# Kernel tuning notes

Measured on AMD Instinct MI355X. Metric: run time of the kernel, lower is better.

The kernel has to match this reference:

```python
import jax, jax.numpy as jnp
import numpy as np

N, E, IN_DIM, HID, TOWERS, NG = 20000, 320000, 16, 50, 5, 64
FO = HID // TOWERS  # out channels per tower = 10
EPS_BN = 1e-5
EPS_STD = 1e-5  # PyG StdAggregation: sqrt(relu(var) + 1e-5)


def setup_inputs() -> dict:
    key = jax.random.key(0)
    ks = jax.random.split(key, 24)
    rn = lambda k, shape: jax.random.normal(k, shape, dtype=jnp.float32) * 0.1
    F0, F1 = IN_DIM, HID
    return {
        "x": jax.random.normal(ks[0], (N, IN_DIM), dtype=jnp.float32),
        "edge_index": jax.random.randint(ks[1], (2, E), 0, N),
        "batch": jnp.sort(jax.random.randint(ks[2], (N,), 0, NG)),
        # conv0: pre Linear(2*F0 -> F0) per tower, post Linear(13*F0 -> FO) per tower, lin Linear(HID->HID)
        "pre_W0": rn(ks[3], (TOWERS, F0, 2 * F0)), "pre_b0": rn(ks[4], (TOWERS, F0)),
        "post_W0": rn(ks[5], (TOWERS, FO, 13 * F0)), "post_b0": rn(ks[6], (TOWERS, FO)),
        "lin_W0": rn(ks[7], (HID, HID)), "lin_b0": rn(ks[8], (HID,)),
        "gamma0": jnp.ones((HID,), jnp.float32), "beta0": jnp.zeros((HID,), jnp.float32),
        # conv1
        "pre_W1": rn(ks[9], (TOWERS, F1, 2 * F1)), "pre_b1": rn(ks[10], (TOWERS, F1)),
        "post_W1": rn(ks[11], (TOWERS, FO, 13 * F1)), "post_b1": rn(ks[12], (TOWERS, FO)),
        "lin_W1": rn(ks[13], (HID, HID)), "lin_b1": rn(ks[14], (HID,)),
        "gamma1": jnp.ones((HID,), jnp.float32), "beta1": jnp.zeros((HID,), jnp.float32),
        # head MLP: HID->50->25->1
        "mlp_W1": rn(ks[15], (50, HID)), "mlp_b1": rn(ks[16], (50,)),
        "mlp_W2": rn(ks[17], (25, 50)), "mlp_b2": rn(ks[18], (25,)),
        "mlp_W3": rn(ks[19], (1, 25)), "mlp_b3": rn(ks[20], (1,)),
    }


def pna_conv(x, src, dst, deg, avg_log, pre_W, pre_b, post_W, post_b, lin_W, lin_b):
    # x: [N, F]; divide_input=False -> every tower sees the full F features.
    n, Fi = x.shape
    T = pre_W.shape[0]
    # message: h = cat([x_i, x_j]) = cat([x[dst], x[src]]), then per-tower pre-MLP (1 Linear)
    h = jnp.concatenate([x[dst], x[src]], axis=-1)                  # [E, 2F]
    hs = jnp.einsum('ef,tgf->etg', h, pre_W) + pre_b                # [E, T, F]
    flat = hs.reshape(hs.shape[0], T * Fi)                          # [E, T*F]
    # multi-aggregation: mean / min / max / std, scattered to dst
    s = jax.ops.segment_sum(flat, dst, num_segments=n)
    s2 = jax.ops.segment_sum(flat * flat, dst, num_segments=n)
    mn = jax.ops.segment_min(flat, dst, num_segments=n)
    mx = jax.ops.segment_max(flat, dst, num_segments=n)
    degc = jnp.maximum(deg, 1.0)[:, None]
    mean = s / degc
    var = s2 / degc - mean * mean
    std = jnp.sqrt(jax.nn.relu(var) + EPS_STD)
    has = (deg > 0)[:, None]
    mn = jnp.where(has, mn, 0.0)
    mx = jnp.where(has, mx, 0.0)
    agg = jnp.concatenate([mean.reshape(n, T, Fi), mn.reshape(n, T, Fi),
                           mx.reshape(n, T, Fi), std.reshape(n, T, Fi)], axis=-1)  # [N,T,4F]
    # degree scalers: identity, amplification, attenuation
    amp = (jnp.log(jnp.maximum(deg, 1.0) + 1.0) / avg_log)[:, None, None]
    out = jnp.concatenate([jnp.broadcast_to(x[:, None, :], (n, T, Fi)),
                           agg, agg * amp, agg / amp], axis=-1)      # [N, T, 13F]
    out = jnp.einsum('ntf,tgf->ntg', out, post_W) + post_b          # [N, T, FO]
    return out.reshape(n, T * post_W.shape[1]) @ lin_W.T + lin_b    # [N, HID]


def _bn_relu(h, g, b):
    mu = h.mean(axis=0)
    v = jnp.mean((h - mu) ** 2, axis=0)  # biased var, torch BN training-mode normalization
    return jax.nn.relu(g * (h - mu) / jnp.sqrt(v + EPS_BN) + b)


def reference(x, edge_index, batch,
              pre_W0, pre_b0, post_W0, post_b0, lin_W0, lin_b0, gamma0, beta0,
              pre_W1, pre_b1, post_W1, post_b1, lin_W1, lin_b1, gamma1, beta1,
              mlp_W1, mlp_b1, mlp_W2, mlp_b2, mlp_W3, mlp_b3):
    src, dst = edge_index[0], edge_index[1]
    n = x.shape[0]
    deg = jax.ops.segment_sum(jnp.ones((src.shape[0],), jnp.float32), dst, num_segments=n)
    avg_log = jnp.mean(jnp.log(deg + 1.0))  # PNA avg_deg['log'] from this graph's degree histogram
    # NOTE: zip(convs, batch_norms) in the torch forward applies only num_conv_layer=2 convs.
    h = pna_conv(x, src, dst, deg, avg_log, pre_W0, pre_b0, post_W0, post_b0, lin_W0, lin_b0)
    h = _bn_relu(h, gamma0, beta0)
    h = pna_conv(h, src, dst, deg, avg_log, pre_W1, pre_b1, post_W1, post_b1, lin_W1, lin_b1)
    h = _bn_relu(h, gamma1, beta1)
    cnt = jax.ops.segment_sum(jnp.ones((n,), jnp.float32), batch, num_segments=NG)
    pooled = jax.ops.segment_sum(h, batch, num_segments=NG) / jnp.maximum(cnt, 1.0)[:, None]
    h = jax.nn.relu(pooled @ mlp_W1.T + mlp_b1)
    h = jax.nn.relu(h @ mlp_W2.T + mlp_b2)
    return h @ mlp_W3.T + mlp_b3  # [NG, 1]
```

## Files before the change

kernel.cpp:

```cpp
#include <hip/hip_runtime.h>
#include <math.h>
#include <float.h>

#define NN 20000
#define EE 320000
#define INDIM 16
#define HID 50
#define TW 5
#define FO 10
#define NGROUPS 64

typedef float f4 __attribute__((ext_vector_type(4)));
typedef float f2 __attribute__((ext_vector_type(2)));

__device__ inline f4 f4_min(f4 a, f4 b) {
    f4 r; r.x = fminf(a.x, b.x); r.y = fminf(a.y, b.y);
    r.z = fminf(a.z, b.z); r.w = fmaxf(-a.w, -b.w) * -1.0f;
    r.w = fminf(a.w, b.w); return r;
}
__device__ inline f4 f4_max(f4 a, f4 b) {
    f4 r; r.x = fmaxf(a.x, b.x); r.y = fmaxf(a.y, b.y);
    r.z = fmaxf(a.z, b.z); r.w = fmaxf(a.w, b.w); return r;
}
__device__ inline float sh3sum(float v, int g0, int G_) {
    return v + __shfl(v, g0 + G_, 64) + __shfl(v, g0 + 2 * G_, 64);
}
__device__ inline float sh3min(float v, int g0, int G_) {
    return fminf(fminf(v, __shfl(v, g0 + G_, 64)), __shfl(v, g0 + 2 * G_, 64));
}
__device__ inline float sh3max(float v, int g0, int G_) {
    return fmaxf(fmaxf(v, __shfl(v, g0 + G_, 64)), __shfl(v, g0 + 2 * G_, 64));
}
__device__ inline void acc4(float& acc, f4 w, float a0, float a1, float a2, float a3) {
    acc += w.x * a0; acc += w.y * a1; acc += w.z * a2; acc += w.w * a3;
}

__global__ void k_deg(const int* __restrict__ dst, int* __restrict__ deg) {
    int e = blockIdx.x * 256 + threadIdx.x;
    if (e < EE) atomicAdd(&deg[dst[e]], 1);
}

__global__ void k_scan(const int* __restrict__ deg, int* __restrict__ offsets,
                       float* __restrict__ scal) {
    __shared__ int part[1024];
    __shared__ float fred[1024];
    const int CH = 20;
    int tid = threadIdx.x;
    int base = tid * CH;
    int loc[CH];
    int s = 0; float fs = 0.f;
    for (int c = 0; c < CH; ++c) {
        int idx = base + c;
        int v = (idx < NN) ? deg[idx] : 0;
        loc[c] = s; s += v;
        if (idx < NN) fs += logf((float)v + 1.0f);
    }
    part[tid] = s; fred[tid] = fs; __syncthreads();
    for (int off = 1; off < 1024; off <<= 1) {
        int v = (tid >= off) ? part[tid - off] : 0;
        __syncthreads();
        part[tid] += v;
        __syncthreads();
    }
    int pre = (tid > 0) ? part[tid - 1] : 0;
    for (int c = 0; c < CH; ++c) {
        int idx = base + c;
        if (idx < NN) offsets[idx] = pre + loc[c];
    }
    if (tid == 0) offsets[NN] = part[1023];
    for (int off = 512; off > 0; off >>= 1) {
        if (tid < off) fred[tid] += fred[tid + off];
        __syncthreads();
    }
    if (tid == 0) scal[0] = fred[0] / (float)NN;
}

__global__ void k_fill(const int* __restrict__ src, const int* __restrict__ dst,
                       const int* __restrict__ offsets, int* __restrict__ cursor,
                       int* __restrict__ csr_src) {
    int e = blockIdx.x * 256 + threadIdx.x;
    if (e < EE) {
        int d = dst[e];
        int pos = offsets[d] + atomicAdd(&cursor[d], 1);
        csr_src[pos] = src[e];
    }
}

__global__ void k_pack(const float* __restrict__ preW0, const float* __restrict__ preW1,
                       const float* __restrict__ postW0, const float* __restrict__ postW1,
                       const float* __restrict__ linW0, const float* __restrict__ linW1,
                       float* __restrict__ preWt0, float* __restrict__ preWt1,
                       float* __restrict__ Wx0, float* __restrict__ Wid0,
                       float* __restrict__ Wamp0, float* __restrict__ Watt0,
                       float* __restrict__ Wx1, float* __restrict__ Wid1,
                       float* __restrict__ Wamp1, float* __restrict__ Watt1,
                       float* __restrict__ Lt0, float* __restrict__ Lt1) {
    int idx = blockIdx.x * 256 + threadIdx.x;
    int job = blockIdx.y;
    int q = idx >> 8, k = (idx >> 2) & 63, j = idx & 3;
    switch (job) {
    case 0:
        if (idx < 32 * 80) { int c = idx / 80, r = idx % 80; preWt0[idx] = preW0[r * 32 + c]; }
        break;
    case 1:
        if (idx < 100 * 256) { int c = idx / 256, r = idx % 256; preWt1[idx] = (r < 250) ? preW1[r * 100 + c] : 0.f; }
        break;
    case 2:
        if (idx < 4 * 256) { int f = q * 4 + j; Wx0[idx] = (k < HID) ? postW0[k * 208 + f] : 0.f; }
        break;
    case 3:
        if (idx < 16 * 256) { int s = q / 4, f = (q % 4) * 4 + j; Wid0[idx] = (k < HID) ? postW0[k * 208 + (1 + s) * 16 + f] : 0.f; }
        break;
    case 4:
        if (idx < 16 * 256) { int s = q / 4, f = (q % 4) * 4 + j; Wamp0[idx] = (k < HID) ? postW0[k * 208 + (5 + s) * 16 + f] : 0.f; }
        break;
    case 5:
        if (idx < 16 * 256) { int s = q / 4, f = (q % 4) * 4 + j; Watt0[idx] = (k < HID) ? postW0[k * 208 + (9 + s) * 16 + f] : 0.f; }
        break;
    case 6:
        if (idx < 13 * 256) { int f = q * 4 + j; Wx1[idx] = (f < 50 && k < HID) ? postW1[k * 650 + f] : 0.f; }
        break;
    case 7:
        if (idx < 52 * 256) { int s = q / 13, f = (q % 13) * 4 + j; Wid1[idx] = (f < 50 && k < HID) ? postW1[k * 650 + (1 + s) * 50 + f] : 0.f; }
        break;
    case 8:
        if (idx < 52 * 256) { int s = q / 13, f = (q % 13) * 4 + j; Wamp1[idx] = (f < 50 && k < HID) ? postW1[k * 650 + (5 + s) * 50 + f] : 0.f; }
        break;
    case 9:
        if (idx < 52 * 256) { int s = q / 13, f = (q % 13) * 4 + j; Watt1[idx] = (f < 50 && k < HID) ? postW1[k * 650 + (9 + s) * 50 + f] : 0.f; }
        break;
    case 10:
        if (idx < 13 * 256) { int f = q * 4 + j; Lt0[idx] = (f < 50 && k < HID) ? linW0[k * 50 + f] : 0.f; }
        break;
    case 11:
        if (idx < 13 * 256) { int f = q * 4 + j; Lt1[idx] = (f < 50 && k < HID) ? linW1[k * 50 + f] : 0.f; }
        break;
    }
}

template <int F, int TF, int TFP>
__global__ __launch_bounds__(256, 4) void k_gemm_CP(
    const float* __restrict__ x, const float* __restrict__ preWt,
    const float* __restrict__ b,
    float* __restrict__ C, float* __restrict__ P) {
    const int NODES = 16;
    __shared__ float xs[NODES * F];
    int tid = threadIdx.x;
    int base = blockIdx.x * NODES;
    for (int idx = tid; idx < NODES * F; idx += 256) xs[idx] = x[(size_t)base * F + idx];
    __syncthreads();
    if (tid < TF) {
        float accC[NODES], accP[NODES];
#pragma unroll
        for (int n = 0; n < NODES; ++n) { accC[n] = 0.f; accP[n] = 0.f; }
        for (int f = 0; f < F; ++f) {
            float wl = preWt[f * TFP + tid];
            float wr = preWt[(F + f) * TFP + tid];
#pragma unroll
            for (int n = 0; n < NODES; ++n) {
                float xv = xs[n * F + f];
                accC[n] += xv * wl;
                accP[n] += xv * wr;
            }
        }
        float bb = b[tid];
        for (int n = 0; n < NODES; ++n) {
            C[((size_t)(base + n)) * TFP + tid] = accC[n] + bb;
            P[((size_t)(base + n)) * TFP + tid] = accP[n];
        }
    } else if (tid < TFP) {
        for (int n = 0; n < NODES; ++n) {
            C[((size_t)(base + n)) * TFP + tid] = 0.f;
            P[((size_t)(base + n)) * TFP + tid] = 0.f;
        }
    }
}

template <int F, int TFP, int EP, int SEGP>
__global__ __launch_bounds__(256, 3) void k_conv(
    const float* __restrict__ xin, const float* __restrict__ C, const float* __restrict__ P,
    const int* __restrict__ offsets, const int* __restrict__ csr,
    const float* __restrict__ scal,
    const float* __restrict__ Wx, const float* __restrict__ Wid,
    const float* __restrict__ Wamp, const float* __restrict__ Watt,
    const float* __restrict__ postb,
    const float* __restrict__ Lt, const float* __restrict__ linb,
    float* __restrict__ hout) {
    const int NB = 8;
    const int G = TFP / 4;
    const int SQ = SEGP / 4;
    __shared__ __align__(16) float sAgg[NB][5][TFP];
    __shared__ __align__(16) float sY[NB][56];
    __shared__ float samp[NB][2];
    int t = threadIdx.x;
    int w = t >> 6, lane = t & 63;
    int ibase = blockIdx.x * NB + 2 * w;

    for (int nn = 0; nn < 2; ++nn) {
        int nd = 2 * w + nn;
        int i = ibase + nn;
        int beg = offsets[i], end = offsets[i + 1];
        int d = end - beg;
        int g = (EP == 1) ? lane : (lane % G);
        int e = (EP == 1) ? 0 : (lane / G);
        bool act = (EP == 1) ? (g < G) : (e < EP);
        f4 S = {0.f, 0.f, 0.f, 0.f}, S2 = {0.f, 0.f, 0.f, 0.f};
        f4 MN = {FLT_MAX, FLT_MAX, FLT_MAX, FLT_MAX};
        f4 MX = {-FLT_MAX, -FLT_MAX, -FLT_MAX, -FLT_MAX};
        const f4* __restrict__ Pv = (const f4*)P;
        if (act) {
            if (EP == 1) {
                int j = beg;
                for (; j + 4 <= end; j += 4) {
                    int s0 = csr[j], s1 = csr[j + 1], s2 = csr[j + 2], s3 = csr[j + 3];
                    f4 a = Pv[(size_t)s0 * G + g];
                    f4 b = Pv[(size_t)s1 * G + g];
                    f4 c = Pv[(size_t)s2 * G + g];
                    f4 dd = Pv[(size_t)s3 * G + g];
                    S += a; S2 += a * a; MN = f4_min(MN, a); MX = f4_max(MX, a);
                    S += b; S2 += b * b; MN = f4_min(MN, b); MX = f4_max(MX, b);
                    S += c; S2 += c * c; MN = f4_min(MN, c); MX = f4_max(MX, c);
                    S += dd; S2 += dd * dd; MN = f4_min(MN, dd); MX = f4_max(MX, dd);
                }
                for (; j < end; ++j) {
                    int s0 = csr[j];
                    f4 a = Pv[(size_t)s0 * G + g];
                    S += a; S2 += a * a; MN = f4_min(MN, a); MX = f4_max(MX, a);
                }
            } else {
                int j = beg + e;
                for (; j + EP < end; j += 2 * EP) {
                    int s0 = csr[j], s1 = csr[j + EP];
                    f4 a = Pv[(size_t)s0 * G + g];
                    f4 b = Pv[(size_t)s1 * G + g];
                    S += a; S2 += a * a; MN = f4_min(MN, a); MX = f4_max(MX, a);
                    S += b; S2 += b * b; MN = f4_min(MN, b); MX = f4_max(MX, b);
                }
                if (j < end) {
                    int s0 = csr[j];
                    f4 a = Pv[(size_t)s0 * G + g];
                    S += a; S2 += a * a; MN = f4_min(MN, a); MX = f4_max(MX, a);
                }
            }
        }
        if (EP == 3) {
            int g0 = lane % G;
            S.x = sh3sum(S.x, g0, G); S.y = sh3sum(S.y, g0, G);
            S.z = sh3sum(S.z, g0, G); S.w = sh3sum(S.w, g0, G);
            S2.x = sh3sum(S2.x, g0, G); S2.y = sh3sum(S2.y, g0, G);
            S2.z = sh3sum(S2.z, g0, G); S2.w = sh3sum(S2.w, g0, G);
            MN.x = sh3min(MN.x, g0, G); MN.y = sh3min(MN.y, g0, G);
            MN.z = sh3min(MN.z, g0, G); MN.w = sh3min(MN.w, g0, G);
            MX.x = sh3max(MX.x, g0, G); MX.y = sh3max(MX.y, g0, G);
            MX.z = sh3max(MX.z, g0, G); MX.w = sh3max(MX.w, g0, G);
        }
        if (lane < G) {
            f4 Cv = ((const f4*)C)[(size_t)i * G + lane];
            float degf = (float)d;
            float rdegc = 1.0f / fmaxf(degf, 1.0f);
            f4 mean, sq, var, stdv, mnv, mxv;
            mean.x = (degf * Cv.x + S.x) * rdegc; mean.y = (degf * Cv.y + S.y) * rdegc;
            mean.z = (degf * Cv.z + S.z) * rdegc; mean.w = (degf * Cv.w + S.w) * rdegc;
            sq.x = degf * Cv.x * Cv.x + 2.f * Cv.x * S.x + S2.x;
            sq.y = degf * Cv.y * Cv.y + 2.f * Cv.y * S.y + S2.y;
            sq.z = degf * Cv.z * Cv.z + 2.f * Cv.z * S.z + S2.z;
            sq.w = degf * Cv.w * Cv.w + 2.f * Cv.w * S.w + S2.w;
            var.x = sq.x * rdegc - mean.x * mean.x; var.y = sq.y * rdegc - mean.y * mean.y;
            var.z = sq.z * rdegc - mean.z * mean.z; var.w = sq.w * rdegc - mean.w * mean.w;
            stdv.x = sqrtf(fmaxf(var.x, 0.f) + 1e-5f); stdv.y = sqrtf(fmaxf(var.y, 0.f) + 1e-5f);
            stdv.z = sqrtf(fmaxf(var.z, 0.f) + 1e-5f); stdv.w = sqrtf(fmaxf(var.w, 0.f) + 1e-5f);
            if (d > 0) {
                mnv.x = Cv.x + MN.x; mnv.y = Cv.y + MN.y; mnv.z = Cv.z + MN.z; mnv.w = Cv.w + MN.w;
                mxv.x = Cv.x + MX.x; mxv.y = Cv.y + MX.y; mxv.z = Cv.z + MX.z; mxv.w = Cv.w + MX.w;
            } else {
                mnv = (f4){0.f, 0.f, 0.f, 0.f}; mxv = mnv;
            }
            ((f4*)&sAgg[nd][0][0])[lane] = mean;
            ((f4*)&sAgg[nd][1][0])[lane] = mnv;
            ((f4*)&sAgg[nd][2][0])[lane] = mxv;
            ((f4*)&sAgg[nd][3][0])[lane] = stdv;
        }
        if (lane < F) sAgg[nd][4][lane] = xin[(size_t)i * F + lane];
        else if (lane < SEGP) sAgg[nd][4][lane] = 0.f;
        if (lane == 0) {
            float amp = logf(fmaxf((float)d, 1.f) + 1.f) / scal[0];
            samp[nd][0] = amp; samp[nd][1] = 1.f / amp;
        }
    }
    __syncthreads();

    int nd0 = 2 * w, nd1 = 2 * w + 1;
    int i0 = ibase, i1 = ibase + 1;
    int k = lane;
    int kk = (k < HID) ? k : (HID - 1);
    int tw = kk / FO;
    const f4* __restrict__ Wxv = (const f4*)Wx;
    const f4* __restrict__ Wiv = (const f4*)Wid;
    const f4* __restrict__ Wav = (const f4*)Wamp;
    const f4* __restrict__ Wtv = (const f4*)Watt;
    float y0a = 0.f, y1a = 0.f, y2a = 0.f, y0b = 0.f, y1b = 0.f, y2b = 0.f;

    const float* __restrict__ A0x = &sAgg[nd0][4][0];
    const float* __restrict__ A1x = &sAgg[nd1][4][0];
#pragma unroll
    for (int q = 0; q < SQ; ++q) {
        f4 wv = Wxv[q * 64 + k];
        f4 a0 = *(const f4*)(A0x + q * 4);
        f4 a1 = *(const f4*)(A1x + q * 4);
        acc4(y0a, wv, a0.x, a0.y, a0.z, a0.w);
        acc4(y0b, wv, a1.x, a1.y, a1.z, a1.w);
    }
#pragma unroll
    for (int s = 0; s < 4; ++s) {
        const float* __restrict__ A0 = &sAgg[nd0][s][tw * F];
        const float* __restrict__ A1 = &sAgg[nd1][s][tw * F];
#pragma unroll 4
        for (int fq = 0; fq < SQ; ++fq) {
            int q = s * SQ + fq;
            f4 wi = Wiv[q * 64 + k];
            f4 wa = Wav[q * 64 + k];
            f4 wt = Wtv[q * 64 + k];
            float a00, a01, a02, a03, a10, a11, a12, a13;
            if constexpr (F % 4 == 0) {
                f4 v0 = *(const f4*)(A0 + fq * 4);
                f4 v1 = *(const f4*)(A1 + fq * 4);
                a00 = v0.x; a01 = v0.y; a02 = v0.z; a03 = v0.w;
                a10 = v1.x; a11 = v1.y; a12 = v1.z; a13 = v1.w;
            } else {
                f2 p0 = *(const f2*)(A0 + fq * 4);
                f2 p1 = *(const f2*)(A0 + fq * 4 + 2);
                f2 q0 = *(const f2*)(A1 + fq * 4);
                f2 q1 = *(const f2*)(A1 + fq * 4 + 2);
                a00 = p0.x; a01 = p0.y; a02 = p1.x; a03 = p1.y;
                a10 = q0.x; a11 = q0.y; a12 = q1.x; a13 = q1.y;
            }
            acc4(y0a, wi, a00, a01, a02, a03);
            acc4(y1a, wa, a00, a01, a02, a03);
            acc4(y2a, wt, a00, a01, a02, a03);
            acc4(y0b, wi, a10, a11, a12, a13);
            acc4(y1b, wa, a10, a11, a12, a13);
            acc4(y2b, wt, a10, a11, a12, a13);
        }
    }
    float ya = postb[kk] + y0a + samp[nd0][0] * y1a + samp[nd0][1] * y2a;
    float yb = postb[kk] + y0b + samp[nd1][0] * y1b + samp[nd1][1] * y2b;
    if (lane < 56) {
        sY[nd0][lane] = (lane < HID) ? ya : 0.f;
        sY[nd1][lane] = (lane < HID) ? yb : 0.f;
    }

    const f4* __restrict__ Lv = (const f4*)Lt;
    float oa = linb[kk], ob = oa;
#pragma unroll
    for (int q = 0; q < 13; ++q) {
        f4 lv = Lv[q * 64 + k];
        f4 s0 = *(const f4*)(&sY[nd0][q * 4]);
        f4 s1 = *(const f4*)(&sY[nd1][q * 4]);
        acc4(oa, lv, s0.x, s0.y, s0.z, s0.w);
        acc4(ob, lv, s1.x, s1.y, s1.z, s1.w);
    }
    if (lane < HID) {
        hout[(size_t)i0 * HID + lane] = oa;
        hout[(size_t)i1 * HID + lane] = ob;
    }
}

__global__ void k_bn_part(const float* __restrict__ h, float* __restrict__ acc) {
    __shared__ float ss[4][64], ss2[4][64];
    int t = threadIdx.x;
    int rs = t >> 6, c = t & 63;
    float s = 0.f, s2 = 0.f;
    if (c < HID) {
        int r0 = blockIdx.x * 200 + rs;
        int rend = blockIdx.x * 200 + 200;
        if (rend > NN) rend = NN;
        for (int r = r0; r < rend; r += 4) {
            float v = h[(size_t)r * HID + c];
            s += v; s2 += v * v;
        }
    }
    ss[rs][c] = s; ss2[rs][c] = s2;
    __syncthreads();
    if (t < HID) {
        float S = ss[0][t] + ss[1][t] + ss[2][t] + ss[3][t];
        float S2 = ss2[0][t] + ss2[1][t] + ss2[2][t] + ss2[3][t];
        atomicAdd(&acc[t], S);
        atomicAdd(&acc[64 + t], S2);
    }
}

__global__ void k_bn_relu(const float* __restrict__ hin, const float* __restrict__ acc,
                          const float* __restrict__ gamma, const float* __restrict__ beta,
                          float* __restrict__ hout) {
    int idx = blockIdx.x * 256 + threadIdx.x;
    if (idx < NN * HID) {
        int c = idx % HID;
        float mu = acc[c] * (1.f / NN);
        float var = acc[64 + c] * (1.f / NN) - mu * mu;
        float v = hin[idx];
        hout[idx] = fmaxf(gamma[c] * (v - mu) * rsqrtf(var + 1e-5f) + beta[c], 0.f);
    }
}

__global__ void k_head(const float* __restrict__ h, const int* __restrict__ batch,
                       const float* __restrict__ W1, const float* __restrict__ b1,
                       const float* __restrict__ W2, const float* __restrict__ b2,
                       const float* __restrict__ W3, const float* __restrict__ b3,
                       float* __restrict__ out) {
    __shared__ float sp[HID], h1[50], h2[25];
    __shared__ int sbound[2];
    int g = blockIdx.x, tid = threadIdx.x;
    if (tid < 2) {
        int target = g + tid;
        int lo = 0, hi = NN;
        while (lo < hi) {
            int mid = (lo + hi) >> 1;
            if (batch[mid] < target) lo = mid + 1; else hi = mid;
        }
        sbound[tid] = lo;
    }
    __syncthreads();
    int beg = sbound[0], end = sbound[1];
    if (tid < HID) {
        float s0 = 0.f, s1 = 0.f, s2 = 0.f, s3 = 0.f;
        int n = beg;
        for (; n + 4 <= end; n += 4) {
            s0 += h[(size_t)n * HID + tid];
            s1 += h[(size_t)(n + 1) * HID + tid];
            s2 += h[(size_t)(n + 2) * HID + tid];
            s3 += h[(size_t)(n + 3) * HID + tid];
        }
        for (; n < end; ++n) s0 += h[(size_t)n * HID + tid];
        sp[tid] = (s0 + s1 + s2 + s3) / fmaxf((float)(end - beg), 1.0f);
    }
    __syncthreads();
    if (tid < 50) {
        float a = b1[tid];
        for (int k = 0; k < HID; ++k) a += W1[tid * HID + k] * sp[k];
        h1[tid] = fmaxf(a, 0.f);
    }
    __syncthreads();
    if (tid < 25) {
        float a = b2[tid];
        for (int k = 0; k < 50; ++k) a += W2[tid * 50 + k] * h1[k];
        h2[tid] = fmaxf(a, 0.f);
    }
    __syncthreads();
    if (tid == 0) {
        float a = b3[0];
        for (int k = 0; k < 25; ++k) a += W3[k] * h2[k];
        out[g] = a;
    }
}

extern "C" void kernel_launch(void* const* d_in, const int* in_sizes, int n_in,
                              void* d_out, int out_size, void* d_ws, size_t ws_size,
                              hipStream_t stream) {
    const float* x      = (const float*)d_in[0];
    const int*   ei     = (const int*)d_in[1];
    const int*   batch  = (const int*)d_in[2];
    const float* preW0  = (const float*)d_in[3];
    const float* preb0  = (const float*)d_in[4];
    const float* postW0 = (const float*)d_in[5];
    const float* postb0 = (const float*)d_in[6];
    const float* linW0  = (const float*)d_in[7];
    const float* linb0  = (const float*)d_in[8];
    const float* gamma0 = (const float*)d_in[9];
    const float* beta0  = (const float*)d_in[10];
    const float* preW1  = (const float*)d_in[11];
    const float* preb1  = (const float*)d_in[12];
    const float* postW1 = (const float*)d_in[13];
    const float* postb1 = (const float*)d_in[14];
    const float* linW1  = (const float*)d_in[15];
    const float* linb1  = (const float*)d_in[16];
    const float* gamma1 = (const float*)d_in[17];
    const float* beta1  = (const float*)d_in[18];
    const float* mW1    = (const float*)d_in[19];
    const float* mb1    = (const float*)d_in[20];
    const float* mW2    = (const float*)d_in[21];
    const float* mb2    = (const float*)d_in[22];
    const float* mW3    = (const float*)d_in[23];
    const float* mb3    = (const float*)d_in[24];
    float* out = (float*)d_out;
    (void)in_sizes; (void)n_in; (void)out_size; (void)ws_size;

    char* ws = (char*)d_ws;
    size_t off = 0;
    auto alloc = [&](size_t bytes) -> void* {
        void* p = ws + off;
        off += (bytes + 255) & ~(size_t)255;
        return p;
    };
    int*   deg     = (int*)alloc((size_t)NN * 4);
    int*   offsets = (int*)alloc((size_t)(NN + 1) * 4);
    int*   cursor  = (int*)alloc((size_t)NN * 4);
    int*   csr_src = (int*)alloc((size_t)EE * 4);
    float* scal    = (float*)alloc(64);
    float* bnacc0  = (float*)alloc(128 * 4);
    float* bnacc1  = (float*)alloc(128 * 4);
    float* preWt0  = (float*)alloc((size_t)32 * 80 * 4);
    float* preWt1  = (float*)alloc((size_t)100 * 256 * 4);
    float* Wx0     = (float*)alloc((size_t)4 * 256 * 4);
    float* Wid0    = (float*)alloc((size_t)16 * 256 * 4);
    float* Wamp0   = (float*)alloc((size_t)16 * 256 * 4);
    float* Watt0   = (float*)alloc((size_t)16 * 256 * 4);
    float* Wx1     = (float*)alloc((size_t)13 * 256 * 4);
    float* Wid1    = (float*)alloc((size_t)52 * 256 * 4);
    float* Wamp1   = (float*)alloc((size_t)52 * 256 * 4);
    float* Watt1   = (float*)alloc((size_t)52 * 256 * 4);
    float* Lt0     = (float*)alloc((size_t)13 * 256 * 4);
    float* Lt1     = (float*)alloc((size_t)13 * 256 * 4);
    float* Cbuf    = (float*)alloc((size_t)NN * 256 * 4);
    float* Pbuf    = (float*)alloc((size_t)NN * 256 * 4);
    float* h1buf   = (float*)alloc((size_t)NN * HID * 4);
    float* h2buf   = (float*)alloc((size_t)NN * HID * 4);

    const int* src = ei;
    const int* dst = ei + EE;

    hipMemsetAsync(deg, 0, (size_t)NN * 4, stream);
    hipMemsetAsync(cursor, 0, (size_t)NN * 4, stream);
    hipMemsetAsync(bnacc0, 0, 128 * 4, stream);
    hipMemsetAsync(bnacc1, 0, 128 * 4, stream);

    k_pack<<<dim3(100, 12), 256, 0, stream>>>(preW0, preW1, postW0, postW1, linW0, linW1,
                                              preWt0, preWt1, Wx0, Wid0, Wamp0, Watt0,
                                              Wx1, Wid1, Wamp1, Watt1, Lt0, Lt1);
    k_deg<<<EE / 256, 256, 0, stream>>>(dst, deg);
    k_scan<<<1, 1024, 0, stream>>>(deg, offsets, scal);
    k_fill<<<EE / 256, 256, 0, stream>>>(src, dst, offsets, cursor, csr_src);

    k_gemm_CP<INDIM, 80, 80><<<NN / 16, 256, 0, stream>>>(x, preWt0, preb0, Cbuf, Pbuf);
    k_conv<INDIM, 80, 3, 16><<<NN / 8, 256, 0, stream>>>(
        x, Cbuf, Pbuf, offsets, csr_src, scal, Wx0, Wid0, Wamp0, Watt0, postb0, Lt0, linb0, h1buf);
    k_bn_part<<<100, 256, 0, stream>>>(h1buf, bnacc0);
    k_bn_relu<<<(NN * HID + 255) / 256, 256, 0, stream>>>(h1buf, bnacc0, gamma0, beta0, h1buf);

    k_gemm_CP<HID, 250, 256><<<NN / 16, 256, 0, stream>>>(h1buf, preWt1, preb1, Cbuf, Pbuf);
    k_conv<HID, 256, 1, 52><<<NN / 8, 256, 0, stream>>>(
        h1buf, Cbuf, Pbuf, offsets, csr_src, scal, Wx1, Wid1, Wamp1, Watt1, postb1, Lt1, linb1, h2buf);
    k_bn_part<<<100, 256, 0, stream>>>(h2buf, bnacc1);
    k_bn_relu<<<(NN * HID + 255) / 256, 256, 0, stream>>>(h2buf, bnacc1, gamma1, beta1, h2buf);

    k_head<<<NGROUPS, 64, 0, stream>>>(h2buf, batch, mW1, mb1, mW2, mb2, mW3, mb3, out);
}
```

Measured before the change: 324.9 us.

## Split fused conv into gather and post kernels with 8-node register blocking

The fused per-node conv kernel becomes two kernels. A gather kernel writes the mean/min/max/std aggregates, plus a padded copy of x for layer 1, to a global buffer. A post kernel then runs the post-MLP and linear layer over 8 nodes per wave, so each loaded weight vector is reused across 8 nodes instead of 2. This cuts repeated weight loads and lets the gather kernel run at higher occupancy without the large shared-memory footprint. The cost is an extra global round trip of the aggregate buffer, about 82 MB for layer 1, plus one more launch per layer.

Measured after the change: 384.6 us. 18.4% more time.

```diff
diff --git a/kernel.cpp b/kernel.cpp
--- a/kernel.cpp
+++ b/kernel.cpp
@@ -15,8 +15,7 @@
 
 __device__ inline f4 f4_min(f4 a, f4 b) {
     f4 r; r.x = fminf(a.x, b.x); r.y = fminf(a.y, b.y);
-    r.z = fminf(a.z, b.z); r.w = fmaxf(-a.w, -b.w) * -1.0f;
-    r.w = fminf(a.w, b.w); return r;
+    r.z = fminf(a.z, b.z); r.w = fminf(a.w, b.w); return r;
 }
 __device__ inline f4 f4_max(f4 a, f4 b) {
     f4 r; r.x = fmaxf(a.x, b.x); r.y = fmaxf(a.y, b.y);
@@ -176,192 +175,187 @@
     }
 }
 
-template <int F, int TFP, int EP, int SEGP>
-__global__ __launch_bounds__(256, 3) void k_conv(
+template <int F, int TFP, int EP, int XSTR>
+__global__ __launch_bounds__(256) void k_gather(
     const float* __restrict__ xin, const float* __restrict__ C, const float* __restrict__ P,
     const int* __restrict__ offsets, const int* __restrict__ csr,
-    const float* __restrict__ scal,
+    float* __restrict__ agg, float* __restrict__ xp) {
+    const int G = TFP / 4;
+    int t = threadIdx.x;
+    int w = t >> 6, lane = t & 63;
+    int i = blockIdx.x * 4 + w;
+    int beg = offsets[i], end = offsets[i + 1];
+    int d = end - beg;
+    int g = (EP == 1) ? lane : (lane % G);
+    int e = (EP == 1) ? 0 : (lane / G);
+    bool act = (EP == 1) ? (g < G) : (e < EP);
+    f4 S = {0.f, 0.f, 0.f, 0.f}, S2 = {0.f, 0.f, 0.f, 0.f};
+    f4 MN = {FLT_MAX, FLT_MAX, FLT_MAX, FLT_MAX};
+    f4 MX = {-FLT_MAX, -FLT_MAX, -FLT_MAX, -FLT_MAX};
+    const f4* __restrict__ Pv = (const f4*)P;
+    if (act) {
+        if (EP == 1) {
+            int j = beg;
+            for (; j + 4 <= end; j += 4) {
+                int s0 = csr[j], s1 = csr[j + 1], s2 = csr[j + 2], s3 = csr[j + 3];
+                f4 a = Pv[(size_t)s0 * G + g];
+                f4 b = Pv[(size_t)s1 * G + g];
+                f4 c = Pv[(size_t)s2 * G + g];
+                f4 dd = Pv[(size_t)s3 * G + g];
+                S += a; S2 += a * a; MN = f4_min(MN, a); MX = f4_max(MX, a);
+                S += b; S2 += b * b; MN = f4_min(MN, b); MX = f4_max(MX, b);
+                S += c; S2 += c * c; MN = f4_min(MN, c); MX = f4_max(MX, c);
+                S += dd; S2 += dd * dd; MN = f4_min(MN, dd); MX = f4_max(MX, dd);
+            }
+            for (; j < end; ++j) {
+                int s0 = csr[j];
+                f4 a = Pv[(size_t)s0 * G + g];
+                S += a; S2 += a * a; MN = f4_min(MN, a); MX = f4_max(MX, a);
+            }
+        } else {
+            int j = beg + e;
+            for (; j + EP < end; j += 2 * EP) {
+                int s0 = csr[j], s1 = csr[j + EP];
+                f4 a = Pv[(size_t)s0 * G + g];
+                f4 b = Pv[(size_t)s1 * G + g];
+                S += a; S2 += a * a; MN = f4_min(MN, a); MX = f4_max(MX, a);
+                S += b; S2 += b * b; MN = f4_min(MN, b); MX = f4_max(MX, b);
+            }
+            if (j < end) {
+                int s0 = csr[j];
+                f4 a = Pv[(size_t)s0 * G + g];
+                S += a; S2 += a * a; MN = f4_min(MN, a); MX = f4_max(MX, a);
+            }
+        }
+    }
+    if (EP == 3) {
+        int g0 = lane % G;
+        S.x = sh3sum(S.x, g0, G); S.y = sh3sum(S.y, g0, G);
+        S.z = sh3sum(S.z, g0, G); S.w = sh3sum(S.w, g0, G);
+        S2.x = sh3sum(S2.x, g0, G); S2.y = sh3sum(S2.y, g0, G);
+        S2.z = sh3sum(S2.z, g0, G); S2.w = sh3sum(S2.w, g0, G);
+        MN.x = sh3min(MN.x, g0, G); MN.y = sh3min(MN.y, g0, G);
+        MN.z = sh3min(MN.z, g0, G); MN.w = sh3min(MN.w, g0, G);
+        MX.x = sh3max(MX.x, g0, G); MX.y = sh3max(MX.y, g0, G);
+        MX.z = sh3max(MX.z, g0, G); MX.w = sh3max(MX.w, g0, G);
+    }
+    if (lane < G) {
+        f4 Cv = ((const f4*)C)[(size_t)i * G + lane];
+        float degf = (float)d;
+        float rdegc = 1.0f / fmaxf(degf, 1.0f);
+        f4 mean, sq, var, stdv, mnv, mxv;
+        mean.x = (degf * Cv.x + S.x) * rdegc; mean.y = (degf * Cv.y + S.y) * rdegc;
+        mean.z = (degf * Cv.z + S.z) * rdegc; mean.w = (degf * Cv.w + S.w) * rdegc;
+        sq.x = degf * Cv.x * Cv.x + 2.f * Cv.x * S.x + S2.x;
+        sq.y = degf * Cv.y * Cv.y + 2.f * Cv.y * S.y + S2.y;
+        sq.z = degf * Cv.z * Cv.z + 2.f * Cv.z * S.z + S2.z;
+        sq.w = degf * Cv.w * Cv.w + 2.f * Cv.w * S.w + S2.w;
+        var.x = sq.x * rdegc - mean.x * mean.x; var.y = sq.y * rdegc - mean.y * mean.y;
+        var.z = sq.z * rdegc - mean.z * mean.z; var.w = sq.w * rdegc - mean.w * mean.w;
+        stdv.x = sqrtf(fmaxf(var.x, 0.f) + 1e-5f); stdv.y = sqrtf(fmaxf(var.y, 0.f) + 1e-5f);
+        stdv.z = sqrtf(fmaxf(var.z, 0.f) + 1e-5f); stdv.w = sqrtf(fmaxf(var.w, 0.f) + 1e-5f);
+        if (d > 0) {
+            mnv.x = Cv.x + MN.x; mnv.y = Cv.y + MN.y; mnv.z = Cv.z + MN.z; mnv.w = Cv.w + MN.w;
+            mxv.x = Cv.x + MX.x; mxv.y = Cv.y + MX.y; mxv.z = Cv.z + MX.z; mxv.w = Cv.w + MX.w;
+        } else {
+            mnv = (f4){0.f, 0.f, 0.f, 0.f}; mxv = mnv;
+        }
+        f4* __restrict__ dstv = (f4*)(agg + (size_t)i * 4 * TFP);
+        dstv[lane] = mean;
+        dstv[G + lane] = mnv;
+        dstv[2 * G + lane] = mxv;
+        dstv[3 * G + lane] = stdv;
+    }
+    if (XSTR > 0 && lane < XSTR)
+        xp[(size_t)i * XSTR + lane] = (lane < F) ? xin[(size_t)i * F + lane] : 0.f;
+}
+
+template <int F, int TFP, int SQ, int SQX, int XSTR, bool AF4>
+__global__ __launch_bounds__(128) void k_post(
+    const float* __restrict__ xsrc, const float* __restrict__ agg,
+    const int* __restrict__ offsets, const float* __restrict__ scal,
     const float* __restrict__ Wx, const float* __restrict__ Wid,
     const float* __restrict__ Wamp, const float* __restrict__ Watt,
     const float* __restrict__ postb,
     const float* __restrict__ Lt, const float* __restrict__ linb,
     float* __restrict__ hout) {
-    const int NB = 8;
-    const int G = TFP / 4;
-    const int SQ = SEGP / 4;
-    __shared__ __align__(16) float sAgg[NB][5][TFP];
-    __shared__ __align__(16) float sY[NB][56];
-    __shared__ float samp[NB][2];
+    __shared__ __align__(16) float sY[2][8][52];
     int t = threadIdx.x;
     int w = t >> 6, lane = t & 63;
-    int ibase = blockIdx.x * NB + 2 * w;
-
-    for (int nn = 0; nn < 2; ++nn) {
-        int nd = 2 * w + nn;
-        int i = ibase + nn;
-        int beg = offsets[i], end = offsets[i + 1];
-        int d = end - beg;
-        int g = (EP == 1) ? lane : (lane % G);
-        int e = (EP == 1) ? 0 : (lane / G);
-        bool act = (EP == 1) ? (g < G) : (e < EP);
-        f4 S = {0.f, 0.f, 0.f, 0.f}, S2 = {0.f, 0.f, 0.f, 0.f};
-        f4 MN = {FLT_MAX, FLT_MAX, FLT_MAX, FLT_MAX};
-        f4 MX = {-FLT_MAX, -FLT_MAX, -FLT_MAX, -FLT_MAX};
-        const f4* __restrict__ Pv = (const f4*)P;
-        if (act) {
-            if (EP == 1) {
-                int j = beg;
-                for (; j + 4 <= end; j += 4) {
-                    int s0 = csr[j], s1 = csr[j + 1], s2 = csr[j + 2], s3 = csr[j + 3];
-                    f4 a = Pv[(size_t)s0 * G + g];
-                    f4 b = Pv[(size_t)s1 * G + g];
-                    f4 c = Pv[(size_t)s2 * G + g];
-                    f4 dd = Pv[(size_t)s3 * G + g];
-                    S += a; S2 += a * a; MN = f4_min(MN, a); MX = f4_max(MX, a);
-                    S += b; S2 += b * b; MN = f4_min(MN, b); MX = f4_max(MX, b);
-                    S += c; S2 += c * c; MN = f4_min(MN, c); MX = f4_max(MX, c);
-                    S += dd; S2 += dd * dd; MN = f4_min(MN, dd); MX = f4_max(MX, dd);
-                }
-                for (; j < end; ++j) {
-                    int s0 = csr[j];
-                    f4 a = Pv[(size_t)s0 * G + g];
-                    S += a; S2 += a * a; MN = f4_min(MN, a); MX = f4_max(MX, a);
-                }
-            } else {
-                int j = beg + e;
-                for (; j + EP < end; j += 2 * EP) {
-                    int s0 = csr[j], s1 = csr[j + EP];
-                    f4 a = Pv[(size_t)s0 * G + g];
-                    f4 b = Pv[(size_t)s1 * G + g];
-                    S += a; S2 += a * a; MN = f4_min(MN, a); MX = f4_max(MX, a);
-                    S += b; S2 += b * b; MN = f4_min(MN, b); MX = f4_max(MX, b);
-                }
-                if (j < end) {
-                    int s0 = csr[j];
-                    f4 a = Pv[(size_t)s0 * G + g];
-                    S += a; S2 += a * a; MN = f4_min(MN, a); MX = f4_max(MX, a);
-                }
-            }
-        }
-        if (EP == 3) {
-            int g0 = lane % G;
-            S.x = sh3sum(S.x, g0, G); S.y = sh3sum(S.y, g0, G);
-            S.z = sh3sum(S.z, g0, G); S.w = sh3sum(S.w, g0, G);
-            S2.x = sh3sum(S2.x, g0, G); S2.y = sh3sum(S2.y, g0, G);
-            S2.z = sh3sum(S2.z, g0, G); S2.w = sh3sum(S2.w, g0, G);
-            MN.x = sh3min(MN.x, g0, G); MN.y = sh3min(MN.y, g0, G);
-            MN.z = sh3min(MN.z, g0, G); MN.w = sh3min(MN.w, g0, G);
-            MX.x = sh3max(MX.x, g0, G); MX.y = sh3max(MX.y, g0, G);
-            MX.z = sh3max(MX.z, g0, G); MX.w = sh3max(MX.w, g0, G);
-        }
-        if (lane < G) {
-            f4 Cv = ((const f4*)C)[(size_t)i * G + lane];
-            float degf = (float)d;
-            float rdegc = 1.0f / fmaxf(degf, 1.0f);
-            f4 mean, sq, var, stdv, mnv, mxv;
-            mean.x = (degf * Cv.x + S.x) * rdegc; mean.y = (degf * Cv.y + S.y) * rdegc;
-            mean.z = (degf * Cv.z + S.z) * rdegc; mean.w = (degf * Cv.w + S.w) * rdegc;
-            sq.x = degf * Cv.x * Cv.x + 2.f * Cv.x * S.x + S2.x;
-            sq.y = degf * Cv.y * Cv.y + 2.f * Cv.y * S.y + S2.y;
-            sq.z = degf * Cv.z * Cv.z + 2.f * Cv.z * S.z + S2.z;
-            sq.w = degf * Cv.w * Cv.w + 2.f * Cv.w * S.w + S2.w;
-            var.x = sq.x * rdegc - mean.x * mean.x; var.y = sq.y * rdegc - mean.y * mean.y;
-            var.z = sq.z * rdegc - mean.z * mean.z; var.w = sq.w * rdegc - mean.w * mean.w;
-            stdv.x = sqrtf(fmaxf(var.x, 0.f) + 1e-5f); stdv.y = sqrtf(fmaxf(var.y, 0.f) + 1e-5f);
-            stdv.z = sqrtf(fmaxf(var.z, 0.f) + 1e-5f); stdv.w = sqrtf(fmaxf(var.w, 0.f) + 1e-5f);
-            if (d > 0) {
-                mnv.x = Cv.x + MN.x; mnv.y = Cv.y + MN.y; mnv.z = Cv.z + MN.z; mnv.w = Cv.w + MN.w;
-                mxv.x = Cv.x + MX.x; mxv.y = Cv.y + MX.y; mxv.z = Cv.z + MX.z; mxv.w = Cv.w + MX.w;
-            } else {
-                mnv = (f4){0.f, 0.f, 0.f, 0.f}; mxv = mnv;
-            }
-            ((f4*)&sAgg[nd][0][0])[lane] = mean;
-            ((f4*)&sAgg[nd][1][0])[lane] = mnv;
-            ((f4*)&sAgg[nd][2][0])[lane] = mxv;
-            ((f4*)&sAgg[nd][3][0])[lane] = stdv;
-        }
-        if (lane < F) sAgg[nd][4][lane] = xin[(size_t)i * F + lane];
-        else if (lane < SEGP) sAgg[nd][4][lane] = 0.f;
-        if (lane == 0) {
-            float amp = logf(fmaxf((float)d, 1.f) + 1.f) / scal[0];
-            samp[nd][0] = amp; samp[nd][1] = 1.f / amp;
-        }
-    }
-    __syncthreads();
-
-    int nd0 = 2 * w, nd1 = 2 * w + 1;
-    int i0 = ibase, i1 = ibase + 1;
-    int k = lane;
-    int kk = (k < HID) ? k : (HID - 1);
+    int base = blockIdx.x * 16 + w * 8;
+    int kk = (lane < HID) ? lane : (HID - 1);
     int tw = kk / FO;
+    float rscal = 1.0f / scal[0];
+    float amp[8], ia[8];
+#pragma unroll
+    for (int n = 0; n < 8; ++n) {
+        int dd = offsets[base + n + 1] - offsets[base + n];
+        float a = logf(fmaxf((float)dd, 1.f) + 1.f) * rscal;
+        amp[n] = a; ia[n] = 1.0f / a;
+    }
+    float y0[8], y1[8], y2[8];
+#pragma unroll
+    for (int n = 0; n < 8; ++n) { y0[n] = 0.f; y1[n] = 0.f; y2[n] = 0.f; }
     const f4* __restrict__ Wxv = (const f4*)Wx;
     const f4* __restrict__ Wiv = (const f4*)Wid;
     const f4* __restrict__ Wav = (const f4*)Wamp;
     const f4* __restrict__ Wtv = (const f4*)Watt;
-    float y0a = 0.f, y1a = 0.f, y2a = 0.f, y0b = 0.f, y1b = 0.f, y2b = 0.f;
-
-    const float* __restrict__ A0x = &sAgg[nd0][4][0];
-    const float* __restrict__ A1x = &sAgg[nd1][4][0];
-#pragma unroll
-    for (int q = 0; q < SQ; ++q) {
-        f4 wv = Wxv[q * 64 + k];
-        f4 a0 = *(const f4*)(A0x + q * 4);
-        f4 a1 = *(const f4*)(A1x + q * 4);
-        acc4(y0a, wv, a0.x, a0.y, a0.z, a0.w);
-        acc4(y0b, wv, a1.x, a1.y, a1.z, a1.w);
-    }
-#pragma unroll
+    for (int q = 0; q < SQX; ++q) {
+        f4 wv = Wxv[q * 64 + lane];
+#pragma unroll
+        for (int n = 0; n < 8; ++n) {
+            f4 a = *(const f4*)(xsrc + (size_t)(base + n) * XSTR + 4 * q);
+            acc4(y0[n], wv, a.x, a.y, a.z, a.w);
+        }
+    }
     for (int s = 0; s < 4; ++s) {
-        const float* __restrict__ A0 = &sAgg[nd0][s][tw * F];
-        const float* __restrict__ A1 = &sAgg[nd1][s][tw * F];
-#pragma unroll 4
-        for (int fq = 0; fq < SQ; ++fq) {
-            int q = s * SQ + fq;
-            f4 wi = Wiv[q * 64 + k];
-            f4 wa = Wav[q * 64 + k];
-            f4 wt = Wtv[q * 64 + k];
-            float a00, a01, a02, a03, a10, a11, a12, a13;
-            if constexpr (F % 4 == 0) {
-                f4 v0 = *(const f4*)(A0 + fq * 4);
-                f4 v1 = *(const f4*)(A1 + fq * 4);
-                a00 = v0.x; a01 = v0.y; a02 = v0.z; a03 = v0.w;
-                a10 = v1.x; a11 = v1.y; a12 = v1.z; a13 = v1.w;
-            } else {
-                f2 p0 = *(const f2*)(A0 + fq * 4);
-                f2 p1 = *(const f2*)(A0 + fq * 4 + 2);
-                f2 q0 = *(const f2*)(A1 + fq * 4);
-                f2 q1 = *(const f2*)(A1 + fq * 4 + 2);
-                a00 = p0.x; a01 = p0.y; a02 = p1.x; a03 = p1.y;
-                a10 = q0.x; a11 = q0.y; a12 = q1.x; a13 = q1.y;
+        for (int q = 0; q < SQ; ++q) {
+            f4 wi = Wiv[(s * SQ + q) * 64 + lane];
+            f4 wa = Wav[(s * SQ + q) * 64 + lane];
+            f4 wt = Wtv[(s * SQ + q) * 64 + lane];
+#pragma unroll
+            for (int n = 0; n < 8; ++n) {
+                const float* __restrict__ Ab =
+                    agg + ((size_t)(base + n) * 4 + s) * TFP + tw * F + 4 * q;
+                float a0, a1, a2, a3;
+                if constexpr (AF4) {
+                    f4 av = *(const f4*)Ab;
+                    a0 = av.x; a1 = av.y; a2 = av.z; a3 = av.w;
+                } else {
+                    f2 u = *(const f2*)Ab;
+                    f2 v = *(const f2*)(Ab + 2);
+                    a0 = u.x; a1 = u.y; a2 = v.x; a3 = v.y;
+                }
+                acc4(y0[n], wi, a0, a1, a2, a3);
+                acc4(y1[n], wa, a0, a1, a2, a3);
+                acc4(y2[n], wt, a0, a1, a2, a3);
             }
-            acc4(y0a, wi, a00, a01, a02, a03);
-            acc4(y1a, wa, a00, a01, a02, a03);
-            acc4(y2a, wt, a00, a01, a02, a03);
-            acc4(y0b, wi, a10, a11, a12, a13);
-            acc4(y1b, wa, a10, a11, a12, a13);
-            acc4(y2b, wt, a10, a11, a12, a13);
-        }
-    }
-    float ya = postb[kk] + y0a + samp[nd0][0] * y1a + samp[nd0][1] * y2a;
-    float yb = postb[kk] + y0b + samp[nd1][0] * y1b + samp[nd1][1] * y2b;
-    if (lane < 56) {
-        sY[nd0][lane] = (lane < HID) ? ya : 0.f;
-        sY[nd1][lane] = (lane < HID) ? yb : 0.f;
-    }
-
+        }
+    }
+    float pb = postb[kk];
+#pragma unroll
+    for (int n = 0; n < 8; ++n) {
+        float y = pb + y0[n] + amp[n] * y1[n] + ia[n] * y2[n];
+        if (lane < HID) sY[w][n][lane] = y;
+        else if (lane < 52) sY[w][n][lane] = 0.f;
+    }
     const f4* __restrict__ Lv = (const f4*)Lt;
-    float oa = linb[kk], ob = oa;
-#pragma unroll
+    float o[8];
+    float lb = linb[kk];
+#pragma unroll
+    for (int n = 0; n < 8; ++n) o[n] = lb;
     for (int q = 0; q < 13; ++q) {
-        f4 lv = Lv[q * 64 + k];
-        f4 s0 = *(const f4*)(&sY[nd0][q * 4]);
-        f4 s1 = *(const f4*)(&sY[nd1][q * 4]);
-        acc4(oa, lv, s0.x, s0.y, s0.z, s0.w);
-        acc4(ob, lv, s1.x, s1.y, s1.z, s1.w);
+        f4 lv = Lv[q * 64 + lane];
+#pragma unroll
+        for (int n = 0; n < 8; ++n) {
+            f4 sv = *(const f4*)(&sY[w][n][4 * q]);
+            acc4(o[n], lv, sv.x, sv.y, sv.z, sv.w);
+        }
     }
     if (lane < HID) {
-        hout[(size_t)i0 * HID + lane] = oa;
-        hout[(size_t)i1 * HID + lane] = ob;
+#pragma unroll
+        for (int n = 0; n < 8; ++n)
+            hout[(size_t)(base + n) * HID + lane] = o[n];
     }
 }
 
@@ -514,6 +508,8 @@
     float* Pbuf    = (float*)alloc((size_t)NN * 256 * 4);
     float* h1buf   = (float*)alloc((size_t)NN * HID * 4);
     float* h2buf   = (float*)alloc((size_t)NN * HID * 4);
+    float* aggbuf  = (float*)alloc((size_t)NN * 4 * 256 * 4);
+    float* xp      = (float*)alloc((size_t)NN * 52 * 4);
 
     const int* src = ei;
     const int* dst = ei + EE;
@@ -531,14 +527,18 @@
     k_fill<<<EE / 256, 256, 0, stream>>>(src, dst, offsets, cursor, csr_src);
 
     k_gemm_CP<INDIM, 80, 80><<<NN / 16, 256, 0, stream>>>(x, preWt0, preb0, Cbuf, Pbuf);
-    k_conv<INDIM, 80, 3, 16><<<NN / 8, 256, 0, stream>>>(
-        x, Cbuf, Pbuf, offsets, csr_src, scal, Wx0, Wid0, Wamp0, Watt0, postb0, Lt0, linb0, h1buf);
+    k_gather<INDIM, 80, 3, 0><<<NN / 4, 256, 0, stream>>>(x, Cbuf, Pbuf, offsets, csr_src,
+                                                          aggbuf, xp);
+    k_post<INDIM, 80, 4, 4, 16, true><<<NN / 16, 128, 0, stream>>>(
+        x, aggbuf, offsets, scal, Wx0, Wid0, Wamp0, Watt0, postb0, Lt0, linb0, h1buf);
     k_bn_part<<<100, 256, 0, stream>>>(h1buf, bnacc0);
     k_bn_relu<<<(NN * HID + 255) / 256, 256, 0, stream>>>(h1buf, bnacc0, gamma0, beta0, h1buf);
 
     k_gemm_CP<HID, 250, 256><<<NN / 16, 256, 0, stream>>>(h1buf, preWt1, preb1, Cbuf, Pbuf);
-    k_conv<HID, 256, 1, 52><<<NN / 8, 256, 0, stream>>>(
-        h1buf, Cbuf, Pbuf, offsets, csr_src, scal, Wx1, Wid1, Wamp1, Watt1, postb1, Lt1, linb1, h2buf);
+    k_gather<HID, 256, 1, 52><<<NN / 4, 256, 0, stream>>>(h1buf, Cbuf, Pbuf, offsets, csr_src,
+                                                          aggbuf, xp);
+    k_post<HID, 256, 13, 13, 52, false><<<NN / 16, 128, 0, stream>>>(
+        xp, aggbuf, offsets, scal, Wx1, Wid1, Wamp1, Watt1, postb1, Lt1, linb1, h2buf);
     k_bn_part<<<100, 256, 0, stream>>>(h2buf, bnacc1);
     k_bn_relu<<<(NN * HID + 255) / 256, 256, 0, stream>>>(h2buf, bnacc1, gamma1, beta1, h2buf);
 
```
